# Kernel tuning notes

Measured on AMD Instinct MI355X. Metric: run time of the kernel, lower is better.

## Reference

```python
import jax, jax.numpy as jnp
import numpy as np

T = 2097152  # conversation length (even, per assert in the original forward)


def setup_inputs() -> dict:
    key = jax.random.key(0)
    k0, k1, k2, k3, k4, k5 = jax.random.split(key, 6)
    emission_scores = jax.random.normal(k0, (T, 2), dtype=jnp.float32)
    label = jax.random.randint(k1, (T,), 0, 2)
    who2who_state = jax.random.randint(k2, (T,), 0, 2)
    position_state = jax.random.randint(k3, (T,), 0, 19)
    # first step must use the zero (padding) transition matrix, per the original assert
    who2who_state = who2who_state.at[0].set(2)
    position_state = position_state.at[0].set(19)
    # learned params: matrice_u2s, matrice_s2u stacked; 19 position matrices stacked
    who2who_params = jax.random.normal(k4, (2, 2, 2), dtype=jnp.float32)
    position_params = jax.random.normal(k5, (19, 2, 2), dtype=jnp.float32)
    return dict(emission_scores=emission_scores, label=label,
                who2who_state=who2who_state, position_state=position_state,
                who2who_params=who2who_params, position_params=position_params)


def reference(emission_scores, label, who2who_state, position_state,
              who2who_params, position_params):
    dt = emission_scores.dtype
    pad = jnp.zeros((1, 2, 2), dtype=dt)
    who2who_sub = jnp.concatenate([who2who_params, pad], axis=0)    # [3,2,2]
    position_sub = jnp.concatenate([position_params, pad], axis=0)  # [20,2,2]
    # per-step combined transition matrices (Who2who_PositionCRF): [T,2,2]
    trans = who2who_sub[who2who_state] + position_sub[position_state]

    Tlen = emission_scores.shape[0]
    idx = jnp.arange(Tlen)
    sum_emission = jnp.sum(emission_scores[idx, label])
    # transitions are used for index > 0 with (label[t-1], label[t])
    sum_transition = jnp.sum(trans[1:][jnp.arange(Tlen - 1), label[:-1], label[1:]])
    gold_score = sum_emission + sum_transition

    # CRF forward (partition) recursion: alpha'[j] = logsumexp_i(alpha[i] + em[t,j] + trans[t,i,j])
    def step(alpha, xt):
        em_t, tr_t = xt  # [2], [2,2]
        new_alpha = jax.nn.logsumexp(alpha[:, None] + em_t[None, :] + tr_t, axis=0)
        return new_alpha, None

    alpha0 = jnp.zeros((2,), dtype=dt)
    alpha, _ = jax.lax.scan(step, alpha0, (emission_scores, trans))
    total_score = jax.nn.logsumexp(alpha)

    return jnp.stack([gold_score, total_score])
```

## Files before the change

### kernel.cpp

```cpp
#include <hip/hip_runtime.h>

#define T_LEN   2097152
#define CHUNK   8
#define BLOCK   256
#define NBLK    (T_LEN / (CHUNK * BLOCK))
#define NWAVE   (BLOCK / 64)
#define FINAL_PER (NBLK / 256)

#define LOG2E 1.44269504088896340736f
#define LN2   0.69314718055994530942f

#if __has_builtin(__builtin_amdgcn_exp2f)
__device__ __forceinline__ float fexp2(float x) { return __builtin_amdgcn_exp2f(x); }
#else
__device__ __forceinline__ float fexp2(float x) { return exp2f(x); }
#endif
#if __has_builtin(__builtin_amdgcn_logf)
__device__ __forceinline__ float flog2(float x) { return __builtin_amdgcn_logf(x); }
#else
__device__ __forceinline__ float flog2(float x) { return log2f(x); }
#endif

#if __has_builtin(__builtin_amdgcn_mov_dpp)
#define DPPF(x, C) __int_as_float(__builtin_amdgcn_mov_dpp(__float_as_int(x), (C), 0xF, 0xF, true))
#define DPPI(x, C) __builtin_amdgcn_mov_dpp((x), (C), 0xF, 0xF, true)
#else
#define DPPF(x, C) __shfl_xor((x), ((C) == 0xB1 ? 1 : (C) == 0x4E ? 2 : 8))
#define DPPI(x, C) __shfl_xor((x), ((C) == 0xB1 ? 1 : (C) == 0x4E ? 2 : 8))
#endif

__device__ __forceinline__ void renorm4(float& a, float& b, float& c, float& d, int& e2) {
    float mx = fmaxf(fmaxf(a, b), fmaxf(c, d));
    int ex = (__float_as_int(mx) >> 23) & 0xff;
    float s = __int_as_float((254 - ex) << 23);
    a *= s; b *= s; c *= s; d *= s;
    e2 += ex - 127;
}
__device__ __forceinline__ void renorm1(float& a, int& e2) {
    int ex = (__float_as_int(a) >> 23) & 0xff;
    float s = __int_as_float((254 - ex) << 23);
    a *= s;
    e2 += ex - 127;
}

#define BSTAGE(GF, GI, mval, rn)                                              \
    {                                                                         \
        float Oa = GF(Pa), Ob = GF(Pb), Oc = GF(Pc), Od = GF(Pd);             \
        int   Oe = GI(e2);                                                    \
        g += GF(g);                                                           \
        const bool hi = (lane & (mval)) != 0;                                 \
        float Xa = hi?Oa:Pa, Xb = hi?Ob:Pb, Xc = hi?Oc:Pc, Xd = hi?Od:Pd;     \
        float Ya = hi?Pa:Oa, Yb = hi?Pb:Ob, Yc = hi?Pc:Oc, Yd = hi?Pd:Od;     \
        Pa = Xa*Ya + Xb*Yc;                                                   \
        Pb = Xa*Yb + Xb*Yd;                                                   \
        Pc = Xc*Ya + Xd*Yc;                                                   \
        Pd = Xc*Yb + Xd*Yd;                                                   \
        e2 += Oe;                                                             \
        if (rn) renorm4(Pa, Pb, Pc, Pd, e2);                                  \
    }

#define GF1(x)  DPPF(x, 0xB1)
#define GI1(x)  DPPI(x, 0xB1)
#define GF2(x)  DPPF(x, 0x4E)
#define GI2(x)  DPPI(x, 0x4E)
#define GF8(x)  DPPF(x, 0x128)
#define GI8(x)  DPPI(x, 0x128)
#define GF4(x)  __shfl_xor((x), 4)
#define GF16(x) __shfl_xor((x), 16)
#define GF32(x) __shfl_xor((x), 32)

__device__ __forceinline__ void wave_reduce_lin(float& Pa, float& Pb, float& Pc, float& Pd,
                                                int& e2, float& g, int lane) {
    BSTAGE(GF1,  GI1,   1, false)
    BSTAGE(GF2,  GI2,   2, true)
    BSTAGE(GF4,  GF4,   4, false)
    BSTAGE(GF8,  GI8,   8, true)
    BSTAGE(GF16, GF16, 16, false)
    BSTAGE(GF32, GF32, 32, true)
}

__global__ __launch_bounds__(BLOCK) void crf_partial(
    const float* __restrict__ em,
    const int*   __restrict__ label,
    const int*   __restrict__ wst,
    const int*   __restrict__ pst,
    const float* __restrict__ w2w,
    const float* __restrict__ pos,
    float* __restrict__ outP,
    int*   __restrict__ outE,
    float* __restrict__ outG)
{
    __shared__ float4 combExp[60];
    __shared__ float4 wPs[NWAVE];
    __shared__ int    wEs[NWAVE];
    __shared__ float  wGs[NWAVE];

    const int tid = threadIdx.x;
    if (tid < 60) {
        const int w = tid / 20, p = tid % 20;
        float v0 = 0.f, v1 = 0.f, v2 = 0.f, v3 = 0.f;
        if (w < 2)  { v0 += w2w[w*4+0]; v1 += w2w[w*4+1]; v2 += w2w[w*4+2]; v3 += w2w[w*4+3]; }
        if (p < 19) { v0 += pos[p*4+0]; v1 += pos[p*4+1]; v2 += pos[p*4+2]; v3 += pos[p*4+3]; }
        combExp[tid] = make_float4(fexp2(v0 * LOG2E), fexp2(v1 * LOG2E),
                                   fexp2(v2 * LOG2E), fexp2(v3 * LOG2E));
    }
    __syncthreads();

    const int t0 = (blockIdx.x * BLOCK + tid) * CHUNK;

    const float4* emv = (const float4*)(em + 2 * (size_t)t0);
    float4 E0 = emv[0], E1 = emv[1], E2 = emv[2], E3 = emv[3];
    const int4* lv = (const int4*)(label + t0);
    const int4* wv = (const int4*)(wst   + t0);
    const int4* pv = (const int4*)(pst   + t0);
    int4 L0 = lv[0], L1 = lv[1];
    int4 W0 = wv[0], W1 = wv[1];
    int4 Q0 = pv[0], Q1 = pv[1];
    int prev = (t0 == 0) ? 0 : label[t0 - 1];

    float Pa, Pb, Pc, Pd;
    int   e2 = 0;
    float gEm  = 0.f;
    float gLin = 1.f;
    int   eg   = 0;

    {
        const float e0 = E0.x, e1 = E0.y;
        const float f0 = fexp2(e0 * LOG2E), f1 = fexp2(e1 * LOG2E);
        const float4 X = combExp[W0.x*20 + Q0.x];
        const int l = L0.x;
        gEm += l ? e1 : e0;
        gLin *= prev ? (l ? X.w : X.z) : (l ? X.y : X.x);
        prev = l;
        Pa = X.x * f0;  Pb = X.y * f1;
        Pc = X.z * f0;  Pd = X.w * f1;
    }

#define STEP(e0v, e1v, wI, pI, lI)                                         \
    {                                                                      \
        const float e0 = (e0v), e1 = (e1v);                                \
        const float f0 = fexp2(e0 * LOG2E);                                \
        const float f1 = fexp2(e1 * LOG2E);                                \
        const float4 X = combExp[(wI)*20 + (pI)];                          \
        const int l = (lI);                                                \
        gEm += l ? e1 : e0;                                                \
        gLin *= prev ? (l ? X.w : X.z) : (l ? X.y : X.x);                  \
        prev = l;                                                          \
        float na = (Pa*X.x + Pb*X.z) * f0;                                 \
        float nb = (Pa*X.y + Pb*X.w) * f1;                                 \
        float nc = (Pc*X.x + Pd*X.z) * f0;                                 \
        float nd = (Pc*X.y + Pd*X.w) * f1;                                 \
        Pa = na; Pb = nb; Pc = nc; Pd = nd;                                \
    }

    STEP(E0.z, E0.w, W0.y, Q0.y, L0.y)
    STEP(E1.x, E1.y, W0.z, Q0.z, L0.z)
    STEP(E1.z, E1.w, W0.w, Q0.w, L0.w)
    renorm4(Pa, Pb, Pc, Pd, e2);
    renorm1(gLin, eg);
    STEP(E2.x, E2.y, W1.x, Q1.x, L1.x)
    STEP(E2.z, E2.w, W1.y, Q1.y, L1.y)
    STEP(E3.x, E3.y, W1.z, Q1.z, L1.z)
    STEP(E3.z, E3.w, W1.w, Q1.w, L1.w)
    renorm4(Pa, Pb, Pc, Pd, e2);
#undef STEP

    float g = gEm + ((float)eg + flog2(gLin)) * LN2;

    const int lane = tid & 63;
    wave_reduce_lin(Pa, Pb, Pc, Pd, e2, g, lane);

    const int wid = tid >> 6;
    if (lane == 0) { wPs[wid] = make_float4(Pa, Pb, Pc, Pd); wEs[wid] = e2; wGs[wid] = g; }
    __syncthreads();
    if (tid == 0) {
        float4 q = wPs[0];
        float Ra = q.x, Rb = q.y, Rc = q.z, Rd = q.w;
        int   re = wEs[0];
        float rg = wGs[0];
        #pragma unroll
        for (int w = 1; w < NWAVE; ++w) {
            float4 t = wPs[w];
            float Ca = Ra*t.x + Rb*t.z;
            float Cb = Ra*t.y + Rb*t.w;
            float Cc = Rc*t.x + Rd*t.z;
            float Cd = Rc*t.y + Rd*t.w;
            Ra = Ca; Rb = Cb; Rc = Cc; Rd = Cd;
            re += wEs[w];
            renorm4(Ra, Rb, Rc, Rd, re);
            rg += wGs[w];
        }
        ((float4*)outP)[blockIdx.x] = make_float4(Ra, Rb, Rc, Rd);
        outE[blockIdx.x] = re;
        outG[blockIdx.x] = rg;
    }
}

__global__ __launch_bounds__(256) void crf_final(
    const float* __restrict__ inP,
    const int*   __restrict__ inE,
    const float* __restrict__ inG,
    float* __restrict__ out)
{
    __shared__ float4 wPs[4];
    __shared__ int    wEs[4];
    __shared__ float  wGs[4];

    const int tid  = threadIdx.x;
    const int base = tid * FINAL_PER;

    float4 q = ((const float4*)inP)[base];
    float Pa = q.x, Pb = q.y, Pc = q.z, Pd = q.w;
    int4  ev = ((const int4*)inE)[tid];
    float4 gv = ((const float4*)inG)[tid];
    int   e2 = ev.x + ev.y + ev.z + ev.w;
    float g  = gv.x + gv.y + gv.z + gv.w;
    #pragma unroll
    for (int k = 1; k < FINAL_PER; ++k) {
        float4 r = ((const float4*)inP)[base + k];
        float Ca = Pa*r.x + Pb*r.z;
        float Cb = Pa*r.y + Pb*r.w;
        float Cc = Pc*r.x + Pd*r.z;
        float Cd = Pc*r.y + Pd*r.w;
        Pa = Ca; Pb = Cb; Pc = Cc; Pd = Cd;
    }
    renorm4(Pa, Pb, Pc, Pd, e2);

    const int lane = tid & 63;
    wave_reduce_lin(Pa, Pb, Pc, Pd, e2, g, lane);

    const int wid = tid >> 6;
    if (lane == 0) { wPs[wid] = make_float4(Pa, Pb, Pc, Pd); wEs[wid] = e2; wGs[wid] = g; }
    __syncthreads();
    if (tid == 0) {
        float4 q0 = wPs[0];
        float Ra = q0.x, Rb = q0.y, Rc = q0.z, Rd = q0.w;
        int   re = wEs[0];
        float rg = wGs[0];
        #pragma unroll
        for (int w = 1; w < 4; ++w) {
            float4 t = wPs[w];
            float Ca = Ra*t.x + Rb*t.z;
            float Cb = Ra*t.y + Rb*t.w;
            float Cc = Rc*t.x + Rd*t.z;
            float Cd = Rc*t.y + Rd*t.w;
            Ra = Ca; Rb = Cb; Rc = Cc; Rd = Cd;
            re += wEs[w];
            renorm4(Ra, Rb, Rc, Rd, re);
            rg += wGs[w];
        }
        out[0] = rg;
        out[1] = ((float)re + flog2(Ra + Rb + Rc + Rd)) * LN2;
    }
}

extern "C" void kernel_launch(void* const* d_in, const int* in_sizes, int n_in,
                              void* d_out, int out_size, void* d_ws, size_t ws_size,
                              hipStream_t stream) {
    const float* em    = (const float*)d_in[0];
    const int*   label = (const int*)  d_in[1];
    const int*   wst   = (const int*)  d_in[2];
    const int*   pst   = (const int*)  d_in[3];
    const float* w2w   = (const float*)d_in[4];
    const float* pos   = (const float*)d_in[5];
    float* out = (float*)d_out;

    float* outP = (float*)d_ws;
    int*   outE = (int*)(outP + NBLK * 4);
    float* outG = (float*)(outE + NBLK);

    crf_partial<<<NBLK, BLOCK, 0, stream>>>(em, label, wst, pst, w2w, pos,
                                            outP, outE, outG);
    crf_final<<<1, 256, 0, stream>>>(outP, outE, outG, out);
}
```

Before: 16.70 us.

## Parallelize final reduction across 1024 threads and drop gold-score renormalization

```diff
diff --git a/kernel.cpp b/kernel.cpp
--- a/kernel.cpp
+++ b/kernel.cpp
@@ -5,7 +5,6 @@
 #define BLOCK   256
 #define NBLK    (T_LEN / (CHUNK * BLOCK))
 #define NWAVE   (BLOCK / 64)
-#define FINAL_PER (NBLK / 256)
 
 #define LOG2E 1.44269504088896340736f
 #define LN2   0.69314718055994530942f
@@ -34,12 +33,6 @@
     int ex = (__float_as_int(mx) >> 23) & 0xff;
     float s = __int_as_float((254 - ex) << 23);
     a *= s; b *= s; c *= s; d *= s;
-    e2 += ex - 127;
-}
-__device__ __forceinline__ void renorm1(float& a, int& e2) {
-    int ex = (__float_as_int(a) >> 23) & 0xff;
-    float s = __int_as_float((254 - ex) << 23);
-    a *= s;
     e2 += ex - 127;
 }
 
@@ -122,7 +115,6 @@
     int   e2 = 0;
     float gEm  = 0.f;
     float gLin = 1.f;
-    int   eg   = 0;
 
     {
         const float e0 = E0.x, e1 = E0.y;
@@ -157,7 +149,6 @@
     STEP(E1.x, E1.y, W0.z, Q0.z, L0.z)
     STEP(E1.z, E1.w, W0.w, Q0.w, L0.w)
     renorm4(Pa, Pb, Pc, Pd, e2);
-    renorm1(gLin, eg);
     STEP(E2.x, E2.y, W1.x, Q1.x, L1.x)
     STEP(E2.z, E2.w, W1.y, Q1.y, L1.y)
     STEP(E3.x, E3.y, W1.z, Q1.z, L1.z)
@@ -165,7 +156,7 @@
     renorm4(Pa, Pb, Pc, Pd, e2);
 #undef STEP
 
-    float g = gEm + ((float)eg + flog2(gLin)) * LN2;
+    float g = gEm + flog2(gLin) * LN2;
 
     const int lane = tid & 63;
     wave_reduce_lin(Pa, Pb, Pc, Pd, e2, g, lane);
@@ -196,61 +187,53 @@
     }
 }
 
-__global__ __launch_bounds__(256) void crf_final(
+__global__ __launch_bounds__(1024) void crf_final(
     const float* __restrict__ inP,
     const int*   __restrict__ inE,
     const float* __restrict__ inG,
     float* __restrict__ out)
 {
-    __shared__ float4 wPs[4];
-    __shared__ int    wEs[4];
-    __shared__ float  wGs[4];
+    __shared__ float4 wPs[16];
+    __shared__ int    wEs[16];
+    __shared__ float  wGs[16];
 
     const int tid  = threadIdx.x;
-    const int base = tid * FINAL_PER;
-
-    float4 q = ((const float4*)inP)[base];
+    const int lane = tid & 63;
+    const int wid  = tid >> 6;
+
+    float4 q = ((const float4*)inP)[tid];
     float Pa = q.x, Pb = q.y, Pc = q.z, Pd = q.w;
-    int4  ev = ((const int4*)inE)[tid];
-    float4 gv = ((const float4*)inG)[tid];
-    int   e2 = ev.x + ev.y + ev.z + ev.w;
-    float g  = gv.x + gv.y + gv.z + gv.w;
-    #pragma unroll
-    for (int k = 1; k < FINAL_PER; ++k) {
-        float4 r = ((const float4*)inP)[base + k];
-        float Ca = Pa*r.x + Pb*r.z;
-        float Cb = Pa*r.y + Pb*r.w;
-        float Cc = Pc*r.x + Pd*r.z;
-        float Cd = Pc*r.y + Pd*r.w;
-        Pa = Ca; Pb = Cb; Pc = Cc; Pd = Cd;
-    }
-    renorm4(Pa, Pb, Pc, Pd, e2);
-
-    const int lane = tid & 63;
+    int   e2 = inE[tid];
+    float g  = inG[tid];
+
     wave_reduce_lin(Pa, Pb, Pc, Pd, e2, g, lane);
 
-    const int wid = tid >> 6;
     if (lane == 0) { wPs[wid] = make_float4(Pa, Pb, Pc, Pd); wEs[wid] = e2; wGs[wid] = g; }
     __syncthreads();
-    if (tid == 0) {
-        float4 q0 = wPs[0];
-        float Ra = q0.x, Rb = q0.y, Rc = q0.z, Rd = q0.w;
-        int   re = wEs[0];
-        float rg = wGs[0];
-        #pragma unroll
-        for (int w = 1; w < 4; ++w) {
-            float4 t = wPs[w];
-            float Ca = Ra*t.x + Rb*t.z;
-            float Cb = Ra*t.y + Rb*t.w;
-            float Cc = Rc*t.x + Rd*t.z;
-            float Cd = Rc*t.y + Rd*t.w;
-            Ra = Ca; Rb = Cb; Rc = Cc; Rd = Cd;
-            re += wEs[w];
-            renorm4(Ra, Rb, Rc, Rd, re);
-            rg += wGs[w];
+
+    if (wid == 0) {
+        float Fa = 1.f, Fb = 0.f, Fc = 0.f, Fd = 1.f;
+        int   fe = 0;
+        float fg = 0.f;
+        if (lane < 16) {
+            float4 t = wPs[lane];
+            Fa = t.x; Fb = t.y; Fc = t.z; Fd = t.w;
+            fe = wEs[lane];
+            fg = wGs[lane];
         }
-        out[0] = rg;
-        out[1] = ((float)re + flog2(Ra + Rb + Rc + Rd)) * LN2;
+        {
+            float Pa2 = Fa, Pb2 = Fb, Pc2 = Fc, Pd2 = Fd;
+            int e2f = fe; float gf = fg;
+            {
+                float &Pa = Pa2, &Pb = Pb2, &Pc = Pc2, &Pd = Pd2;
+                int &e2 = e2f; float &g = gf;
+                wave_reduce_lin(Pa, Pb, Pc, Pd, e2, g, lane);
+            }
+            if (lane == 0) {
+                out[0] = gf;
+                out[1] = ((float)e2f + flog2(Pa2 + Pb2 + Pc2 + Pd2)) * LN2;
+            }
+        }
     }
 }
 
@@ -271,5 +254,5 @@
 
     crf_partial<<<NBLK, BLOCK, 0, stream>>>(em, label, wst, pst, w2w, pos,
                                             outP, outE, outG);
-    crf_final<<<1, 256, 0, stream>>>(outP, outE, outG, out);
-}
+    crf_final<<<1, 1024, 0, stream>>>(outP, outE, outG, out);
+}
```

After: 17.31 us. +3.7%, slower.
